# Performance work log

Measured on AMD Instinct MI355X. Metric: run time of the kernel, lower is better.

## Reference

```python
import jax, jax.numpy as jnp
import numpy as np

B, N, FD, D, HF, WF = 4, 6, 256, 128, 64, 120
IMG_H, IMG_W = 480, 960
EPS_LN = 1e-5


def bilinear_sample(fmap, pts):
    """fmap: (B,C,H,W); pts: (B,P,2) xy pixel coords. Returns (B,P,C) values
    (zeros padding, align_corners=True convention) and (B,P) in-bounds mask."""
    Bc, C, H, W = fmap.shape
    flat = fmap.reshape(Bc, C, H * W)
    x, y = pts[..., 0], pts[..., 1]
    x0, y0 = jnp.floor(x), jnp.floor(y)
    out = jnp.zeros((Bc, pts.shape[1], C), fmap.dtype)
    for dx in (0.0, 1.0):
        for dy in (0.0, 1.0):
            cx, cy = x0 + dx, y0 + dy
            wgt = (1.0 - jnp.abs(x - cx)) * (1.0 - jnp.abs(y - cy))
            inb = (cx >= 0) & (cx <= W - 1) & (cy >= 0) & (cy <= H - 1)
            idx = (jnp.clip(cy, 0, H - 1) * W + jnp.clip(cx, 0, W - 1)).astype(jnp.int32)
            g = jnp.take_along_axis(flat, idx[:, None, :], axis=2)  # (B,C,P)
            out = out + (g * (wgt * inb)[:, None, :]).transpose(0, 2, 1)
    valid = (x >= 0) & (x <= W - 1) & (y >= 0) & (y <= H - 1)
    return out, valid


def _l2norm(x, axis):
    n = jnp.sqrt(jnp.sum(x * x, axis=axis, keepdims=True))
    return x / jnp.maximum(n, 1e-12)


def _ln(x, g, b):
    mu = jnp.mean(x, axis=-1, keepdims=True)
    var = jnp.mean((x - mu) ** 2, axis=-1, keepdims=True)
    return (x - mu) / jnp.sqrt(var + EPS_LN) * g + b


def setup_inputs() -> dict:
    key = jax.random.key(0)
    ks = jax.random.split(key, 12)
    rng = np.random.RandomState(0)
    feature = jax.random.normal(ks[0], (B, N, FD, HF, WF), jnp.float32)
    # realistic intrinsics (same K family for src/tar so homographies land in-frame)
    K = np.zeros((B, N, 3, 3), np.float32)
    K[..., 0, 0] = IMG_W * 0.8 * (1 + 0.01 * rng.randn(B, N))
    K[..., 1, 1] = IMG_W * 0.8 * (1 + 0.01 * rng.randn(B, N))
    K[..., 0, 2] = IMG_W / 2
    K[..., 1, 2] = IMG_H / 2
    K[..., 2, 2] = 1.0
    I_tar_inv = np.linalg.inv(K[:, 0]).astype(np.float32)  # (B,3,3)
    # extrinsics: near-identity rotation + small translation
    E = np.tile(np.eye(4, dtype=np.float32), (B, N, 1, 1))
    w = 0.02 * rng.randn(B, N, 3).astype(np.float32)
    skew = np.zeros((B, N, 3, 3), np.float32)
    skew[..., 0, 1], skew[..., 0, 2] = -w[..., 2], w[..., 1]
    skew[..., 1, 0], skew[..., 1, 2] = w[..., 2], -w[..., 0]
    skew[..., 2, 0], skew[..., 2, 1] = -w[..., 1], w[..., 0]
    E[..., :3, :3] = np.eye(3, dtype=np.float32) + skew
    E[..., :3, 3] = 0.1 * rng.randn(B, N, 3).astype(np.float32)
    nv = np.tile(np.array([0.0, -1.0, 0.0], np.float32), (B, 1, 1))
    nv += 0.01 * rng.randn(B, 1, 3).astype(np.float32)
    nv /= np.linalg.norm(nv, axis=-1, keepdims=True)
    sc_in, sc_hid = 1.0 / np.sqrt(FD), 1.0 / np.sqrt(D)
    return {
        "feature": feature,
        "I_src": jnp.asarray(K),
        "I_tar_inv": jnp.asarray(I_tar_inv),
        "E": jnp.asarray(E),
        "dis": jnp.float32(1.5),
        "norm_vec": jnp.asarray(nv),
        "bn_gamma": jnp.ones((FD,), jnp.float32),
        "bn_beta": jnp.zeros((FD,), jnp.float32),
        "bn_mean": jnp.zeros((FD,), jnp.float32),
        "bn_var": jnp.ones((FD,), jnp.float32),
        "conv_w": jax.random.normal(ks[1], (D, FD), jnp.float32) * sc_in,
        "ln1_g": jnp.ones((D,), jnp.float32),
        "ln1_b": jnp.zeros((D,), jnp.float32),
        "mlp_w1": jax.random.normal(ks[2], (D, 2 * D), jnp.float32) * sc_hid,
        "mlp_b1": jnp.zeros((2 * D,), jnp.float32),
        "mlp_w2": jax.random.normal(ks[3], (2 * D, D), jnp.float32) * sc_hid,
        "mlp_b2": jnp.zeros((D,), jnp.float32),
        "ln2_g": jnp.ones((D,), jnp.float32),
        "ln2_b": jnp.zeros((D,), jnp.float32),
    }


def reference(feature, I_src, I_tar_inv, E, dis, norm_vec, bn_gamma, bn_beta,
              bn_mean, bn_var, conv_w, ln1_g, ln1_b, mlp_w1, mlp_b1, mlp_w2,
              mlp_b2, ln2_g, ln2_b):
    b, n, fd, h, w = feature.shape
    d = conv_w.shape[0]
    P = h * w
    # feature_linear: BN (inference stats) + ReLU + 1x1 conv (no bias)
    f = (feature - bn_mean[:, None, None]) / jnp.sqrt(bn_var[:, None, None] + 1e-5)
    f = f * bn_gamma[:, None, None] + bn_beta[:, None, None]
    f = jax.nn.relu(f)
    val = jnp.einsum('of,bnfhw->bnohw', conv_w, f)  # (b,n,d,h,w)
    # homography of normalized grid scaled to image pixels
    xs = jnp.linspace(0.0, 1.0, w)
    ys = jnp.linspace(0.0, 1.0, h)
    X, Y = jnp.meshgrid(xs, ys)  # (h,w), xy indexing
    pix = jnp.stack([X.ravel() * IMG_W, Y.ravel() * IMG_H, jnp.ones(P)], 0)  # (3,P)
    R = E[..., :3, :3]
    T = E[..., :3, 3:]
    Hm = I_src @ (R - (T @ norm_vec[:, None]) / dis) @ I_tar_inv[:, None]  # (b,n,3,3)
    homo = jnp.einsum('bnij,jp->bnip', Hm, pix.astype(Hm.dtype))
    uv = homo[:, :, :2] / homo[:, :, 2:3]
    uv = uv / jnp.array([[IMG_W], [IMG_H]], uv.dtype)  # (b,n,2,P) in ~[0,1]
    # HomoGuideAttention
    pts = (uv * jnp.array([[w], [h]], uv.dtype)).transpose(0, 1, 3, 2).reshape(b * n, P, 2)
    sampled, valid = bilinear_sample(val.reshape(b * n, d, h, w), pts)  # (bn,P,d),(bn,P)
    keyv = _l2norm(sampled, axis=2).reshape(b, n, P, d)
    query = val[:, 0]  # (b,d,h,w)
    q = _l2norm(query.reshape(b, d, P), axis=1)
    dot = jnp.einsum('bdp,bnpd->bnp', q, keyv)
    dot = dot * valid.reshape(b, n, P).astype(dot.dtype)
    att = jax.nn.softmax(dot, axis=1)
    z = jnp.einsum('bnp,bnpd->bpd', att, sampled.reshape(b, n, P, d))
    z = z.transpose(0, 2, 1).reshape(b, d, h, w) + query
    z = z.reshape(b, d, P).transpose(0, 2, 1)  # (b,P,d)
    z = _ln(z, ln1_g, ln1_b)
    hmid = jax.nn.gelu(z @ mlp_w1 + mlp_b1, approximate=False)
    z = z + (hmid @ mlp_w2 + mlp_b2)
    z = _ln(z, ln2_g, ln2_b)
    return z.transpose(0, 2, 1).reshape(b, d, h, w)
```

## Files before the change

kernel.cpp:

```cpp
#include <hip/hip_runtime.h>
#include <hip/hip_bf16.h>
#include <math.h>

#define B_ 4
#define N_ 6
#define FD_ 256
#define D_ 128
#define HF_ 64
#define WF_ 120
#define P_ (HF_*WF_)

typedef __attribute__((ext_vector_type(8))) short short8;
typedef __attribute__((ext_vector_type(4))) float floatx4;
typedef __attribute__((ext_vector_type(4))) unsigned int uint4e;

__device__ inline float gred_sum(float v) {
  v += __shfl_xor(v, 1); v += __shfl_xor(v, 2);
  v += __shfl_xor(v, 4); v += __shfl_xor(v, 8);
  return v;
}

__device__ inline unsigned short f2bf(float f) {
  unsigned int u = __builtin_bit_cast(unsigned int, f);
  u += 0x7fffu + ((u >> 16) & 1u);
  return (unsigned short)(u >> 16);
}
__device__ inline float bf2f(unsigned short h) {
  return __builtin_bit_cast(float, ((unsigned int)h) << 16);
}
__device__ inline void bfu2(unsigned int u, float& lo, float& hi) {
  lo = __builtin_bit_cast(float, u << 16);
  hi = __builtin_bit_cast(float, u & 0xffff0000u);
}

__global__ void prep_kernel(const float* __restrict__ I_src, const float* __restrict__ I_tar_inv,
                            const float* __restrict__ E, const float* __restrict__ dis,
                            const float* __restrict__ norm_vec,
                            const float* __restrict__ bn_gamma, const float* __restrict__ bn_beta,
                            const float* __restrict__ bn_mean, const float* __restrict__ bn_var,
                            float* __restrict__ bnscale, float* __restrict__ bnbias,
                            float* __restrict__ Hm) {
  int t = threadIdx.x;
  if (t < FD_) {
    float s = bn_gamma[t] * rsqrtf(bn_var[t] + 1e-5f);
    bnscale[t] = s;
    bnbias[t] = bn_beta[t] - bn_mean[t] * s;
  }
  if (t < B_*N_) {
    int b = t / N_;
    const float* e = E + t*16;
    const float* nv = norm_vec + b*3;
    float inv_dis = 1.0f / dis[0];
    float M[9];
    #pragma unroll
    for (int r = 0; r < 3; r++)
      #pragma unroll
      for (int c = 0; c < 3; c++)
        M[r*3+c] = e[r*4+c] - e[r*4+3]*nv[c]*inv_dis;
    const float* Is = I_src + t*9;
    float A[9];
    #pragma unroll
    for (int r = 0; r < 3; r++)
      #pragma unroll
      for (int c = 0; c < 3; c++)
        A[r*3+c] = Is[r*3+0]*M[0*3+c] + Is[r*3+1]*M[1*3+c] + Is[r*3+2]*M[2*3+c];
    const float* It = I_tar_inv + b*9;
    #pragma unroll
    for (int r = 0; r < 3; r++)
      #pragma unroll
      for (int c = 0; c < 3; c++)
        Hm[t*9 + r*3+c] = A[r*3+0]*It[0*3+c] + A[r*3+1]*It[1*3+c] + A[r*3+2]*It[2*3+c];
  }
}

__global__ void swizzle_w_kernel(const float* __restrict__ conv_w, unsigned short* __restrict__ wswz) {
  int t = blockIdx.x * 256 + threadIdx.x;
  int j    =  t        & 7;
  int lane = (t >> 3)  & 63;
  int dt   = (t >> 9)  & 7;
  int kc   =  t >> 12;
  int d = dt*16 + (lane & 15);
  int k = kc*32 + (lane >> 4)*8 + j;
  wswz[t] = f2bf(conv_w[d*FD_ + k]);
}

__global__ void swizzle_mlp_kernel(const float* __restrict__ w1, const float* __restrict__ w2,
                                   unsigned short* __restrict__ w1s, unsigned short* __restrict__ w2s) {
  int t = blockIdx.x * 256 + threadIdx.x;
  if (t < 32768) {
    int j    =  t        & 7;
    int lane = (t >> 3)  & 63;
    int dt   = (t >> 9)  & 15;
    int kc   =  t >> 13;
    int n = dt*16 + (lane & 15);
    int k = kc*32 + (lane >> 4)*8 + j;
    w1s[t] = f2bf(w1[k*256 + n]);
  } else {
    int u = t - 32768;
    int j    =  u        & 7;
    int lane = (u >> 3)  & 63;
    int dt   = (u >> 9)  & 7;
    int kc   =  u >> 12;
    int n = dt*16 + (lane & 15);
    int k = kc*32 + (lane >> 4)*8 + j;
    w2s[u] = f2bf(w2[k*128 + n]);
  }
}

__global__ __launch_bounds__(256) void conv_kernel(const float* __restrict__ feature,
    const unsigned short* __restrict__ wswz, const float* __restrict__ bnscale,
    const float* __restrict__ bnbias, unsigned short* __restrict__ val) {
  __shared__ unsigned short apad[2][64*36];
  __shared__ unsigned short ytile[64*136];
  __shared__ float sbn[512];

  int tid = threadIdx.x;
  if (tid < 256) { sbn[tid] = bnscale[tid]; sbn[256+tid] = bnbias[tid]; }

  int bn = blockIdx.y;
  int p0 = blockIdx.x * 64;
  const float* fbase2 = feature + (size_t)bn*FD_*P_ + p0;

  int K0 = tid >> 4;
  int pc = tid & 15;
  int sp = pc*4;

  int ln = tid & 63, wv = tid >> 6;
  int m = ln & 15, q = ln >> 4;
  int row = wv*16 + m;

  auto stage = [&](int kc, int bb) {
    int k0 = kc*32;
    const float* fb = fbase2 + (size_t)(k0 + 2*K0)*P_ + sp;
    float4 v0 = *(const float4*)fb;
    float4 v1 = *(const float4*)(fb + P_);
    float s0 = sbn[k0+2*K0],   b0 = sbn[256+k0+2*K0];
    float s1 = sbn[k0+2*K0+1], b1 = sbn[256+k0+2*K0+1];
    float a0[4] = {v0.x, v0.y, v0.z, v0.w};
    float a1[4] = {v1.x, v1.y, v1.z, v1.w};
    #pragma unroll
    for (int i = 0; i < 4; i++) {
      unsigned int w = (unsigned int)f2bf(fmaxf(a0[i]*s0+b0, 0.f))
                     | ((unsigned int)f2bf(fmaxf(a1[i]*s1+b1, 0.f)) << 16);
      *(unsigned int*)&apad[bb][(sp+i)*36 + 2*K0] = w;
    }
  };

  floatx4 acc[8];
  #pragma unroll
  for (int dt = 0; dt < 8; dt++) acc[dt] = (floatx4){0.f,0.f,0.f,0.f};

  stage(0, 0);
  __syncthreads();

  for (int kc = 0; kc < 8; kc++) {
    int bb = kc & 1;
    if (kc < 7) stage(kc+1, bb ^ 1);
    uint2 u0 = *(const uint2*)&apad[bb][row*36 + q*8];
    uint2 u1 = *(const uint2*)&apad[bb][row*36 + q*8 + 4];
    uint4e ua = {u0.x, u0.y, u1.x, u1.y};
    short8 af = __builtin_bit_cast(short8, ua);
    #pragma unroll
    for (int dt = 0; dt < 8; dt++) {
      short8 bfg = *(const short8*)(wswz + (((size_t)kc*8 + dt)*64 + ln)*8);
      acc[dt] = __builtin_amdgcn_mfma_f32_16x16x32_bf16(af, bfg, acc[dt], 0, 0, 0);
    }
    if (kc < 7) __syncthreads();
  }

  #pragma unroll
  for (int dt = 0; dt < 8; dt++)
    #pragma unroll
    for (int r = 0; r < 4; r++)
      ytile[(wv*16 + q*4 + r)*136 + dt*16 + m] = f2bf(acc[dt][r]);
  __syncthreads();
  #pragma unroll
  for (int i = 0; i < 4; i++) {
    int idx = tid + i*256;
    int pp = idx >> 4, ch = idx & 15;
    uint4 v = *(const uint4*)&ytile[pp*136 + ch*8];
    *(uint4*)(val + ((size_t)bn*P_ + p0 + pp)*D_ + ch*8) = v;
  }
}

__global__ __launch_bounds__(256) void att_kernel(const unsigned short* __restrict__ val,
    const float* __restrict__ Hm, const float* __restrict__ ln1_g,
    const float* __restrict__ ln1_b, unsigned short* __restrict__ zbuf) {
  int b = blockIdx.y;
  int p0 = blockIdx.x * 32;
  int tid = threadIdx.x;
  int ln = tid & 63, wv = tid >> 6;
  int grp = ln >> 4, c = ln & 15;

  float g1[8], be1[8];
  *(float4*)&g1[0]  = *(const float4*)(ln1_g + c*8);
  *(float4*)&g1[4]  = *(const float4*)(ln1_g + c*8 + 4);
  *(float4*)&be1[0] = *(const float4*)(ln1_b + c*8);
  *(float4*)&be1[4] = *(const float4*)(ln1_b + c*8 + 4);

  for (int pi = 0; pi < 2; pi++) {
    int p = p0 + wv*8 + grp*2 + pi;
    int py = p / WF_, px = p - py*WF_;
    float pixx = (float)px * (960.f/119.f);
    float pixy = (float)py * (480.f/63.f);

    const unsigned short* qptr = val + ((size_t)(b*N_)*P_ + p)*D_ + c*8;
    uint4 qu = *(const uint4*)qptr;
    float qv[8];
    bfu2(qu.x, qv[0], qv[1]); bfu2(qu.y, qv[2], qv[3]);
    bfu2(qu.z, qv[4], qv[5]); bfu2(qu.w, qv[6], qv[7]);
    float qp = 0.f;
    #pragma unroll
    for (int i = 0; i < 8; i++) qp += qv[i]*qv[i];
    float qinv = 1.f / fmaxf(sqrtf(gred_sum(qp)), 1e-12f);

    float dotv[N_];
    float sv[N_][8];
    #pragma unroll
    for (int n = 0; n < N_; n++) {
      const float* H = Hm + (b*N_+n)*9;
      float hx = H[0]*pixx + H[1]*pixy + H[2];
      float hy = H[3]*pixx + H[4]*pixy + H[5];
      float hz = H[6]*pixx + H[7]*pixy + H[8];
      float sx = (hx/hz) * ((float)WF_/960.f);
      float sy = (hy/hz) * ((float)HF_/480.f);
      float x0f = floorf(sx), y0f = floorf(sy);
      float fx = sx - x0f, fy = sy - y0f;
      int x0 = (int)x0f, y0 = (int)y0f;
      const unsigned short* base = val + ((size_t)(b*N_+n)*P_)*D_ + c*8;
      float acc[8];
      #pragma unroll
      for (int i = 0; i < 8; i++) acc[i] = 0.f;
      #pragma unroll
      for (int dy = 0; dy < 2; dy++) {
        #pragma unroll
        for (int dx = 0; dx < 2; dx++) {
          int cx = x0 + dx, cy = y0 + dy;
          float wgt = (dx ? fx : 1.f-fx) * (dy ? fy : 1.f-fy);
          bool inb = (cx >= 0) && (cx <= WF_-1) && (cy >= 0) && (cy <= HF_-1);
          int icx = min(max(cx,0),WF_-1), icy = min(max(cy,0),HF_-1);
          uint4 gu = *(const uint4*)(base + (size_t)(icy*WF_ + icx)*D_);
          float g[8];
          bfu2(gu.x, g[0], g[1]); bfu2(gu.y, g[2], g[3]);
          bfu2(gu.z, g[4], g[5]); bfu2(gu.w, g[6], g[7]);
          float wm = inb ? wgt : 0.f;
          #pragma unroll
          for (int i = 0; i < 8; i++) acc[i] += g[i]*wm;
        }
      }
      float ssp = 0.f, qsp = 0.f;
      #pragma unroll
      for (int i = 0; i < 8; i++) { ssp += acc[i]*acc[i]; qsp += qv[i]*acc[i]; }
      float ss = gred_sum(ssp);
      float qs = gred_sum(qsp);
      float dn = qs * qinv / fmaxf(sqrtf(ss), 1e-12f);
      bool valid = (sx >= 0.f) && (sx <= (float)(WF_-1)) && (sy >= 0.f) && (sy <= (float)(HF_-1));
      dotv[n] = valid ? dn : 0.f;
      #pragma unroll
      for (int i = 0; i < 8; i++) sv[n][i] = acc[i];
    }
    float mx = dotv[0];
    #pragma unroll
    for (int n = 1; n < N_; n++) mx = fmaxf(mx, dotv[n]);
    float e[N_]; float den = 0.f;
    #pragma unroll
    for (int n = 0; n < N_; n++) { e[n] = expf(dotv[n]-mx); den += e[n]; }
    float rden = 1.f/den;
    float z[8];
    #pragma unroll
    for (int i = 0; i < 8; i++) z[i] = qv[i];
    #pragma unroll
    for (int n = 0; n < N_; n++) {
      float a = e[n]*rden;
      #pragma unroll
      for (int i = 0; i < 8; i++) z[i] += a*sv[n][i];
    }
    float sp = 0.f;
    #pragma unroll
    for (int i = 0; i < 8; i++) sp += z[i];
    float mu = gred_sum(sp) * (1.f/128.f);
    float vp = 0.f;
    #pragma unroll
    for (int i = 0; i < 8; i++) { float d0 = z[i]-mu; vp += d0*d0; }
    float var = gred_sum(vp) * (1.f/128.f);
    float rs = rsqrtf(var + 1e-5f);
    unsigned int ow[4];
    #pragma unroll
    for (int i = 0; i < 4; i++) {
      float o0 = (z[2*i]-mu)*rs*g1[2*i] + be1[2*i];
      float o1 = (z[2*i+1]-mu)*rs*g1[2*i+1] + be1[2*i+1];
      ow[i] = (unsigned int)f2bf(o0) | ((unsigned int)f2bf(o1) << 16);
    }
    uint4 ov = make_uint4(ow[0], ow[1], ow[2], ow[3]);
    *(uint4*)(zbuf + ((size_t)b*P_ + p)*D_ + c*8) = ov;
  }
}

__global__ __launch_bounds__(256) void mlp_kernel(const unsigned short* __restrict__ zbuf,
    const unsigned short* __restrict__ w1s, const float* __restrict__ b1,
    const unsigned short* __restrict__ w2s, const float* __restrict__ b2,
    const float* __restrict__ ln2_g, const float* __restrict__ ln2_b,
    float* __restrict__ out) {
  __shared__ unsigned short zt[64*136];
  __shared__ unsigned short ht[64*264];
  int tid = threadIdx.x;
  int b = blockIdx.y;
  int p0 = blockIdx.x * 64;

  #pragma unroll
  for (int i = 0; i < 4; i++) {
    int idx = tid + i*256;
    int pp = idx >> 4, ch = idx & 15;
    uint4 v = *(const uint4*)(zbuf + ((size_t)b*P_ + p0 + pp)*D_ + ch*8);
    *(uint4*)&zt[pp*136 + ch*8] = v;
  }
  __syncthreads();

  int ln = tid & 63, wv = tid >> 6;
  int m = ln & 15, q = ln >> 4;

  floatx4 a1[16];
  #pragma unroll
  for (int dt = 0; dt < 16; dt++) a1[dt] = (floatx4){0.f,0.f,0.f,0.f};
  #pragma unroll
  for (int kc = 0; kc < 4; kc++) {
    short8 af = *(const short8*)&zt[(wv*16+m)*136 + kc*32 + q*8];
    #pragma unroll
    for (int dt = 0; dt < 16; dt++) {
      short8 bfg = *(const short8*)(w1s + (((size_t)kc*16 + dt)*64 + ln)*8);
      a1[dt] = __builtin_amdgcn_mfma_f32_16x16x32_bf16(af, bfg, a1[dt], 0, 0, 0);
    }
  }
  #pragma unroll
  for (int dt = 0; dt < 16; dt++) {
    float bb = b1[dt*16 + m];
    #pragma unroll
    for (int r = 0; r < 4; r++) {
      float x = a1[dt][r] + bb;
      float hv = 0.5f*x*(1.f + erff(x*0.70710678118654752f));
      int pp = wv*16 + q*4 + r;
      ht[pp*264 + dt*16 + m] = f2bf(hv);
    }
  }
  __syncthreads();

  floatx4 a2[8];
  #pragma unroll
  for (int dt = 0; dt < 8; dt++) a2[dt] = (floatx4){0.f,0.f,0.f,0.f};
  #pragma unroll
  for (int kc = 0; kc < 8; kc++) {
    short8 af = *(const short8*)&ht[(wv*16+m)*264 + kc*32 + q*8];
    #pragma unroll
    for (int dt = 0; dt < 8; dt++) {
      short8 bfg = *(const short8*)(w2s + (((size_t)kc*8 + dt)*64 + ln)*8);
      a2[dt] = __builtin_amdgcn_mfma_f32_16x16x32_bf16(af, bfg, a2[dt], 0, 0, 0);
    }
  }
  float y[8][4];
  #pragma unroll
  for (int dt = 0; dt < 8; dt++) {
    float bb = b2[dt*16 + m];
    #pragma unroll
    for (int r = 0; r < 4; r++) {
      int pp = wv*16 + q*4 + r;
      y[dt][r] = a2[dt][r] + bb + bf2f(zt[pp*136 + dt*16 + m]);
    }
  }
  float gg[8], be[8];
  #pragma unroll
  for (int dt = 0; dt < 8; dt++) { gg[dt] = ln2_g[dt*16+m]; be[dt] = ln2_b[dt*16+m]; }
  #pragma unroll
  for (int r = 0; r < 4; r++) {
    float sp = 0.f;
    #pragma unroll
    for (int dt = 0; dt < 8; dt++) sp += y[dt][r];
    float mu = gred_sum(sp) * (1.f/128.f);
    float vp = 0.f;
    #pragma unroll
    for (int dt = 0; dt < 8; dt++) { float d0 = y[dt][r]-mu; vp += d0*d0; }
    float rs = rsqrtf(gred_sum(vp) * (1.f/128.f) + 1e-5f);
    #pragma unroll
    for (int dt = 0; dt < 8; dt++) y[dt][r] = (y[dt][r]-mu)*rs*gg[dt] + be[dt];
  }
  __syncthreads();
  float* yt = (float*)ht;
  #pragma unroll
  for (int dt = 0; dt < 8; dt++)
    #pragma unroll
    for (int r = 0; r < 4; r++)
      yt[(dt*16 + m)*66 + wv*16 + q*4 + r] = y[dt][r];
  __syncthreads();

  #pragma unroll
  for (int i = 0; i < 16; i++) {
    int idx = tid + i*256;
    int d = idx >> 5, f2 = idx & 31;
    float2 v = *(float2*)&yt[d*66 + f2*2];
    *(float2*)(out + ((size_t)(b*D_ + d))*P_ + p0 + f2*2) = v;
  }
}

extern "C" void kernel_launch(void* const* d_in, const int* in_sizes, int n_in,
                              void* d_out, int out_size, void* d_ws, size_t ws_size,
                              hipStream_t stream) {
  (void)in_sizes; (void)n_in; (void)out_size; (void)ws_size;
  const float* feature   = (const float*)d_in[0];
  const float* I_src     = (const float*)d_in[1];
  const float* I_tar_inv = (const float*)d_in[2];
  const float* E         = (const float*)d_in[3];
  const float* dis       = (const float*)d_in[4];
  const float* norm_vec  = (const float*)d_in[5];
  const float* bn_gamma  = (const float*)d_in[6];
  const float* bn_beta   = (const float*)d_in[7];
  const float* bn_mean   = (const float*)d_in[8];
  const float* bn_var    = (const float*)d_in[9];
  const float* conv_w    = (const float*)d_in[10];
  const float* ln1_g     = (const float*)d_in[11];
  const float* ln1_b     = (const float*)d_in[12];
  const float* mlp_w1    = (const float*)d_in[13];
  const float* mlp_b1    = (const float*)d_in[14];
  const float* mlp_w2    = (const float*)d_in[15];
  const float* mlp_b2    = (const float*)d_in[16];
  const float* ln2_g     = (const float*)d_in[17];
  const float* ln2_b     = (const float*)d_in[18];
  float* out = (float*)d_out;

  char* ws = (char*)d_ws;
  float* bnscale       = (float*)(ws + 0);
  float* bnbias        = (float*)(ws + 1024);
  float* Hm            = (float*)(ws + 2048);
  unsigned short* wswz = (unsigned short*)(ws + 4096);
  unsigned short* w1s  = (unsigned short*)(ws + 69632);
  unsigned short* w2s  = (unsigned short*)(ws + 135168);
  unsigned short* val  = (unsigned short*)(ws + 200704);
  unsigned short* zbuf = (unsigned short*)(ws + 200704 + 47185920ULL);

  hipLaunchKernelGGL(prep_kernel, dim3(1), dim3(256), 0, stream,
                     I_src, I_tar_inv, E, dis, norm_vec,
                     bn_gamma, bn_beta, bn_mean, bn_var, bnscale, bnbias, Hm);
  hipLaunchKernelGGL(swizzle_w_kernel, dim3(128), dim3(256), 0, stream, conv_w, wswz);
  hipLaunchKernelGGL(swizzle_mlp_kernel, dim3(256), dim3(256), 0, stream,
                     mlp_w1, mlp_w2, w1s, w2s);
  hipLaunchKernelGGL(conv_kernel, dim3(120, 24), dim3(256), 0, stream,
                     feature, wswz, bnscale, bnbias, val);
  hipLaunchKernelGGL(att_kernel, dim3(240, 4), dim3(256), 0, stream,
                     val, Hm, ln1_g, ln1_b, zbuf);
  hipLaunchKernelGGL(mlp_kernel, dim3(120, 4), dim3(256), 0, stream,
                     zbuf, w1s, mlp_b1, w2s, mlp_b2, ln2_g, ln2_b, out);
}
```

Measured before the change: 374.4 us.

## Prefetch conv inputs two stages ahead, precompute sample coords, split MLP tiles

The conv kernel now issues global loads two k-chunks ahead in registers and aliases the output tile with the staging buffers to cut LDS use. A new uv_kernel precomputes the homography sample coordinates so the attention kernel skips per-pixel projective divides, and it batches gathers for two views at a time to raise memory-level parallelism. The MLP kernel uses 32-pixel tiles split across wave pairs, with a cross-wave LayerNorm reduction through shared memory, doubling block count. This adds an extra launch and uv buffer traffic, and uses a one-pass variance formula.

```diff
diff --git a/kernel.cpp b/kernel.cpp
--- a/kernel.cpp
+++ b/kernel.cpp
@@ -71,6 +71,22 @@
       for (int c = 0; c < 3; c++)
         Hm[t*9 + r*3+c] = A[r*3+0]*It[0*3+c] + A[r*3+1]*It[1*3+c] + A[r*3+2]*It[2*3+c];
   }
+}
+
+__global__ void uv_kernel(const float* __restrict__ Hm, float2* __restrict__ uvbuf) {
+  int t = blockIdx.x * 256 + threadIdx.x;
+  int p  = t % P_;
+  int bn = t / P_;
+  int py = p / WF_, px = p - py*WF_;
+  float pixx = (float)px * (960.f/119.f);
+  float pixy = (float)py * (480.f/63.f);
+  const float* H = Hm + bn*9;
+  float hx = H[0]*pixx + H[1]*pixy + H[2];
+  float hy = H[3]*pixx + H[4]*pixy + H[5];
+  float hz = H[6]*pixx + H[7]*pixy + H[8];
+  float sx = (hx/hz) * ((float)WF_/960.f);
+  float sy = (hy/hz) * ((float)HF_/480.f);
+  uvbuf[t] = make_float2(sx, sy);
 }
 
 __global__ void swizzle_w_kernel(const float* __restrict__ conv_w, unsigned short* __restrict__ wswz) {
@@ -107,57 +123,83 @@
   }
 }
 
+#define AST_ 36
 __global__ __launch_bounds__(256) void conv_kernel(const float* __restrict__ feature,
     const unsigned short* __restrict__ wswz, const float* __restrict__ bnscale,
     const float* __restrict__ bnbias, unsigned short* __restrict__ val) {
-  __shared__ unsigned short apad[2][64*36];
-  __shared__ unsigned short ytile[64*136];
-  __shared__ float sbn[512];
+  __shared__ __align__(16) char csm[19968];
+  unsigned short* apadA = (unsigned short*)csm;
+  unsigned short* apadB = (unsigned short*)(csm + 4608);
+  unsigned short* ytile = (unsigned short*)csm;
+  float* sbn = (float*)(csm + 17408);
 
   int tid = threadIdx.x;
-  if (tid < 256) { sbn[tid] = bnscale[tid]; sbn[256+tid] = bnbias[tid]; }
+  sbn[tid] = bnscale[tid]; sbn[256+tid] = bnbias[tid];
 
   int bn = blockIdx.y;
   int p0 = blockIdx.x * 64;
   const float* fbase2 = feature + (size_t)bn*FD_*P_ + p0;
 
   int K0 = tid >> 4;
-  int pc = tid & 15;
-  int sp = pc*4;
+  int sp = (tid & 15) * 4;
 
   int ln = tid & 63, wv = tid >> 6;
   int m = ln & 15, q = ln >> 4;
   int row = wv*16 + m;
 
-  auto stage = [&](int kc, int bb) {
-    int k0 = kc*32;
-    const float* fb = fbase2 + (size_t)(k0 + 2*K0)*P_ + sp;
-    float4 v0 = *(const float4*)fb;
-    float4 v1 = *(const float4*)(fb + P_);
+  float4 va[2], vb[2];
+  {
+    const float* fb0 = fbase2 + (size_t)(2*K0)*P_ + sp;
+    va[0] = *(const float4*)fb0; vb[0] = *(const float4*)(fb0 + P_);
+    const float* fb1 = fbase2 + (size_t)(32 + 2*K0)*P_ + sp;
+    va[1] = *(const float4*)fb1; vb[1] = *(const float4*)(fb1 + P_);
+  }
+  __syncthreads();
+
+  floatx4 acc[8];
+  #pragma unroll
+  for (int dt = 0; dt < 8; dt++) acc[dt] = (floatx4){0.f,0.f,0.f,0.f};
+
+  {
+    int k0 = 0;
     float s0 = sbn[k0+2*K0],   b0 = sbn[256+k0+2*K0];
     float s1 = sbn[k0+2*K0+1], b1 = sbn[256+k0+2*K0+1];
-    float a0[4] = {v0.x, v0.y, v0.z, v0.w};
-    float a1[4] = {v1.x, v1.y, v1.z, v1.w};
+    float a0[4] = {va[0].x, va[0].y, va[0].z, va[0].w};
+    float a1[4] = {vb[0].x, vb[0].y, vb[0].z, vb[0].w};
     #pragma unroll
     for (int i = 0; i < 4; i++) {
       unsigned int w = (unsigned int)f2bf(fmaxf(a0[i]*s0+b0, 0.f))
                      | ((unsigned int)f2bf(fmaxf(a1[i]*s1+b1, 0.f)) << 16);
-      *(unsigned int*)&apad[bb][(sp+i)*36 + 2*K0] = w;
-    }
-  };
-
-  floatx4 acc[8];
-  #pragma unroll
-  for (int dt = 0; dt < 8; dt++) acc[dt] = (floatx4){0.f,0.f,0.f,0.f};
-
-  stage(0, 0);
-  __syncthreads();
-
+      *(unsigned int*)&apadA[(sp+i)*AST_ + 2*K0] = w;
+    }
+  }
+
+  #pragma unroll
   for (int kc = 0; kc < 8; kc++) {
-    int bb = kc & 1;
-    if (kc < 7) stage(kc+1, bb ^ 1);
-    uint2 u0 = *(const uint2*)&apad[bb][row*36 + q*8];
-    uint2 u1 = *(const uint2*)&apad[bb][row*36 + q*8 + 4];
+    __syncthreads();
+    if (kc + 2 < 8) {
+      const float* fb = fbase2 + (size_t)((kc+2)*32 + 2*K0)*P_ + sp;
+      va[kc&1] = *(const float4*)fb;
+      vb[kc&1] = *(const float4*)(fb + P_);
+    }
+    if (kc + 1 < 8) {
+      int s = (kc+1)&1;
+      int k0 = (kc+1)*32;
+      unsigned short* ap = ((kc+1)&1) ? apadB : apadA;
+      float s0 = sbn[k0+2*K0],   b0 = sbn[256+k0+2*K0];
+      float s1 = sbn[k0+2*K0+1], b1 = sbn[256+k0+2*K0+1];
+      float a0[4] = {va[s].x, va[s].y, va[s].z, va[s].w};
+      float a1[4] = {vb[s].x, vb[s].y, vb[s].z, vb[s].w};
+      #pragma unroll
+      for (int i = 0; i < 4; i++) {
+        unsigned int w = (unsigned int)f2bf(fmaxf(a0[i]*s0+b0, 0.f))
+                       | ((unsigned int)f2bf(fmaxf(a1[i]*s1+b1, 0.f)) << 16);
+        *(unsigned int*)&ap[(sp+i)*AST_ + 2*K0] = w;
+      }
+    }
+    unsigned short* rp = (kc&1) ? apadB : apadA;
+    uint2 u0 = *(const uint2*)&rp[row*AST_ + q*8];
+    uint2 u1 = *(const uint2*)&rp[row*AST_ + q*8 + 4];
     uint4e ua = {u0.x, u0.y, u1.x, u1.y};
     short8 af = __builtin_bit_cast(short8, ua);
     #pragma unroll
@@ -165,8 +207,8 @@
       short8 bfg = *(const short8*)(wswz + (((size_t)kc*8 + dt)*64 + ln)*8);
       acc[dt] = __builtin_amdgcn_mfma_f32_16x16x32_bf16(af, bfg, acc[dt], 0, 0, 0);
     }
-    if (kc < 7) __syncthreads();
-  }
+  }
+  __syncthreads();
 
   #pragma unroll
   for (int dt = 0; dt < 8; dt++)
@@ -184,7 +226,7 @@
 }
 
 __global__ __launch_bounds__(256) void att_kernel(const unsigned short* __restrict__ val,
-    const float* __restrict__ Hm, const float* __restrict__ ln1_g,
+    const float2* __restrict__ uvbuf, const float* __restrict__ ln1_g,
     const float* __restrict__ ln1_b, unsigned short* __restrict__ zbuf) {
   int b = blockIdx.y;
   int p0 = blockIdx.x * 32;
@@ -200,12 +242,8 @@
 
   for (int pi = 0; pi < 2; pi++) {
     int p = p0 + wv*8 + grp*2 + pi;
-    int py = p / WF_, px = p - py*WF_;
-    float pixx = (float)px * (960.f/119.f);
-    float pixy = (float)py * (480.f/63.f);
-
-    const unsigned short* qptr = val + ((size_t)(b*N_)*P_ + p)*D_ + c*8;
-    uint4 qu = *(const uint4*)qptr;
+
+    uint4 qu = *(const uint4*)(val + ((size_t)(b*N_)*P_ + p)*D_ + c*8);
     float qv[8];
     bfu2(qu.x, qv[0], qv[1]); bfu2(qu.y, qv[2], qv[3]);
     bfu2(qu.z, qv[4], qv[5]); bfu2(qu.w, qv[6], qv[7]);
@@ -217,47 +255,53 @@
     float dotv[N_];
     float sv[N_][8];
     #pragma unroll
-    for (int n = 0; n < N_; n++) {
-      const float* H = Hm + (b*N_+n)*9;
-      float hx = H[0]*pixx + H[1]*pixy + H[2];
-      float hy = H[3]*pixx + H[4]*pixy + H[5];
-      float hz = H[6]*pixx + H[7]*pixy + H[8];
-      float sx = (hx/hz) * ((float)WF_/960.f);
-      float sy = (hy/hz) * ((float)HF_/480.f);
-      float x0f = floorf(sx), y0f = floorf(sy);
-      float fx = sx - x0f, fy = sy - y0f;
-      int x0 = (int)x0f, y0 = (int)y0f;
-      const unsigned short* base = val + ((size_t)(b*N_+n)*P_)*D_ + c*8;
-      float acc[8];
-      #pragma unroll
-      for (int i = 0; i < 8; i++) acc[i] = 0.f;
-      #pragma unroll
-      for (int dy = 0; dy < 2; dy++) {
+    for (int np = 0; np < 3; np++) {
+      uint4 g[2][4]; float wm[2][4]; bool vld[2];
+      #pragma unroll
+      for (int t = 0; t < 2; t++) {
+        int n = np*2 + t;
+        float2 uv = uvbuf[((size_t)(b*N_ + n))*P_ + p];
+        float sx = uv.x, sy = uv.y;
+        float x0f = floorf(sx), y0f = floorf(sy);
+        float fx = sx - x0f, fy = sy - y0f;
+        int x0 = (int)x0f, y0 = (int)y0f;
+        const unsigned short* base = val + ((size_t)(b*N_+n)*P_)*D_ + c*8;
         #pragma unroll
-        for (int dx = 0; dx < 2; dx++) {
+        for (int k = 0; k < 4; k++) {
+          int dx = k & 1, dy = k >> 1;
           int cx = x0 + dx, cy = y0 + dy;
-          float wgt = (dx ? fx : 1.f-fx) * (dy ? fy : 1.f-fy);
           bool inb = (cx >= 0) && (cx <= WF_-1) && (cy >= 0) && (cy <= HF_-1);
           int icx = min(max(cx,0),WF_-1), icy = min(max(cy,0),HF_-1);
-          uint4 gu = *(const uint4*)(base + (size_t)(icy*WF_ + icx)*D_);
-          float g[8];
-          bfu2(gu.x, g[0], g[1]); bfu2(gu.y, g[2], g[3]);
-          bfu2(gu.z, g[4], g[5]); bfu2(gu.w, g[6], g[7]);
-          float wm = inb ? wgt : 0.f;
+          wm[t][k] = inb ? (dx ? fx : 1.f-fx) * (dy ? fy : 1.f-fy) : 0.f;
+          g[t][k] = *(const uint4*)(base + (size_t)(icy*WF_ + icx)*D_);
+        }
+        vld[t] = (sx >= 0.f) && (sx <= (float)(WF_-1)) && (sy >= 0.f) && (sy <= (float)(HF_-1));
+      }
+      #pragma unroll
+      for (int t = 0; t < 2; t++) {
+        int n = np*2 + t;
+        float acc[8];
+        #pragma unroll
+        for (int i = 0; i < 8; i++) acc[i] = 0.f;
+        #pragma unroll
+        for (int k = 0; k < 4; k++) {
+          float gg[8];
+          bfu2(g[t][k].x, gg[0], gg[1]); bfu2(g[t][k].y, gg[2], gg[3]);
+          bfu2(g[t][k].z, gg[4], gg[5]); bfu2(g[t][k].w, gg[6], gg[7]);
+          float w = wm[t][k];
           #pragma unroll
-          for (int i = 0; i < 8; i++) acc[i] += g[i]*wm;
+          for (int i = 0; i < 8; i++) acc[i] += gg[i]*w;
         }
+        float ssp = 0.f, qsp = 0.f;
+        #pragma unroll
+        for (int i = 0; i < 8; i++) { ssp += acc[i]*acc[i]; qsp += qv[i]*acc[i]; }
+        float ss = gred_sum(ssp);
+        float qs = gred_sum(qsp);
+        float dn = qs * qinv / fmaxf(sqrtf(ss), 1e-12f);
+        dotv[n] = vld[t] ? dn : 0.f;
+        #pragma unroll
+        for (int i = 0; i < 8; i++) sv[n][i] = acc[i];
       }
-      float ssp = 0.f, qsp = 0.f;
-      #pragma unroll
-      for (int i = 0; i < 8; i++) { ssp += acc[i]*acc[i]; qsp += qv[i]*acc[i]; }
-      float ss = gred_sum(ssp);
-      float qs = gred_sum(qsp);
-      float dn = qs * qinv / fmaxf(sqrtf(ss), 1e-12f);
-      bool valid = (sx >= 0.f) && (sx <= (float)(WF_-1)) && (sy >= 0.f) && (sy <= (float)(HF_-1));
-      dotv[n] = valid ? dn : 0.f;
-      #pragma unroll
-      for (int i = 0; i < 8; i++) sv[n][i] = acc[i];
     }
     float mx = dotv[0];
     #pragma unroll
@@ -282,8 +326,7 @@
     float vp = 0.f;
     #pragma unroll
     for (int i = 0; i < 8; i++) { float d0 = z[i]-mu; vp += d0*d0; }
-    float var = gred_sum(vp) * (1.f/128.f);
-    float rs = rsqrtf(var + 1e-5f);
+    float rs = rsqrtf(gred_sum(vp) * (1.f/128.f) + 1e-5f);
     unsigned int ow[4];
     #pragma unroll
     for (int i = 0; i < 4; i++) {
@@ -291,8 +334,7 @@
       float o1 = (z[2*i+1]-mu)*rs*g1[2*i+1] + be1[2*i+1];
       ow[i] = (unsigned int)f2bf(o0) | ((unsigned int)f2bf(o1) << 16);
     }
-    uint4 ov = make_uint4(ow[0], ow[1], ow[2], ow[3]);
-    *(uint4*)(zbuf + ((size_t)b*P_ + p)*D_ + c*8) = ov;
+    *(uint4*)(zbuf + ((size_t)b*P_ + p)*D_ + c*8) = make_uint4(ow[0], ow[1], ow[2], ow[3]);
   }
 }
 
@@ -301,102 +343,124 @@
     const unsigned short* __restrict__ w2s, const float* __restrict__ b2,
     const float* __restrict__ ln2_g, const float* __restrict__ ln2_b,
     float* __restrict__ out) {
-  __shared__ unsigned short zt[64*136];
-  __shared__ unsigned short ht[64*264];
+  __shared__ __align__(16) char smem[26112];
+  unsigned short* zt = (unsigned short*)smem;
+  unsigned short* ht = (unsigned short*)(smem + 8704);
+  float* lnp = (float*)(smem + 25600);
+  float* yt = (float*)smem;
+
   int tid = threadIdx.x;
   int b = blockIdx.y;
-  int p0 = blockIdx.x * 64;
-
-  #pragma unroll
-  for (int i = 0; i < 4; i++) {
+  int p0 = blockIdx.x * 32;
+  int ln = tid & 63, wv = tid >> 6;
+  int m = ln & 15, q = ln >> 4;
+  int h = wv >> 1, ch2 = wv & 1;
+
+  #pragma unroll
+  for (int i = 0; i < 2; i++) {
     int idx = tid + i*256;
     int pp = idx >> 4, ch = idx & 15;
-    uint4 v = *(const uint4*)(zbuf + ((size_t)b*P_ + p0 + pp)*D_ + ch*8);
-    *(uint4*)&zt[pp*136 + ch*8] = v;
-  }
-  __syncthreads();
-
-  int ln = tid & 63, wv = tid >> 6;
-  int m = ln & 15, q = ln >> 4;
-
-  floatx4 a1[16];
-  #pragma unroll
-  for (int dt = 0; dt < 16; dt++) a1[dt] = (floatx4){0.f,0.f,0.f,0.f};
+    *(uint4*)&zt[pp*136 + ch*8] = *(const uint4*)(zbuf + ((size_t)b*P_ + p0 + pp)*D_ + ch*8);
+  }
+  __syncthreads();
+
+  floatx4 a1[8];
+  #pragma unroll
+  for (int j = 0; j < 8; j++) a1[j] = (floatx4){0.f,0.f,0.f,0.f};
   #pragma unroll
   for (int kc = 0; kc < 4; kc++) {
-    short8 af = *(const short8*)&zt[(wv*16+m)*136 + kc*32 + q*8];
-    #pragma unroll
-    for (int dt = 0; dt < 16; dt++) {
+    short8 af = *(const short8*)&zt[(h*16+m)*136 + kc*32 + q*8];
+    #pragma unroll
+    for (int j = 0; j < 8; j++) {
+      int dt = ch2*8 + j;
       short8 bfg = *(const short8*)(w1s + (((size_t)kc*16 + dt)*64 + ln)*8);
-      a1[dt] = __builtin_amdgcn_mfma_f32_16x16x32_bf16(af, bfg, a1[dt], 0, 0, 0);
-    }
-  }
-  #pragma unroll
-  for (int dt = 0; dt < 16; dt++) {
+      a1[j] = __builtin_amdgcn_mfma_f32_16x16x32_bf16(af, bfg, a1[j], 0, 0, 0);
+    }
+  }
+  #pragma unroll
+  for (int j = 0; j < 8; j++) {
+    int dt = ch2*8 + j;
     float bb = b1[dt*16 + m];
     #pragma unroll
     for (int r = 0; r < 4; r++) {
-      float x = a1[dt][r] + bb;
+      float x = a1[j][r] + bb;
       float hv = 0.5f*x*(1.f + erff(x*0.70710678118654752f));
-      int pp = wv*16 + q*4 + r;
-      ht[pp*264 + dt*16 + m] = f2bf(hv);
-    }
-  }
-  __syncthreads();
-
-  floatx4 a2[8];
-  #pragma unroll
-  for (int dt = 0; dt < 8; dt++) a2[dt] = (floatx4){0.f,0.f,0.f,0.f};
+      ht[(h*16 + q*4 + r)*264 + dt*16 + m] = f2bf(hv);
+    }
+  }
+  __syncthreads();
+
+  floatx4 a2[4];
+  #pragma unroll
+  for (int j = 0; j < 4; j++) a2[j] = (floatx4){0.f,0.f,0.f,0.f};
   #pragma unroll
   for (int kc = 0; kc < 8; kc++) {
-    short8 af = *(const short8*)&ht[(wv*16+m)*264 + kc*32 + q*8];
-    #pragma unroll
-    for (int dt = 0; dt < 8; dt++) {
+    short8 af = *(const short8*)&ht[(h*16+m)*264 + kc*32 + q*8];
+    #pragma unroll
+    for (int j = 0; j < 4; j++) {
+      int dt = ch2*4 + j;
       short8 bfg = *(const short8*)(w2s + (((size_t)kc*8 + dt)*64 + ln)*8);
-      a2[dt] = __builtin_amdgcn_mfma_f32_16x16x32_bf16(af, bfg, a2[dt], 0, 0, 0);
-    }
-  }
-  float y[8][4];
-  #pragma unroll
-  for (int dt = 0; dt < 8; dt++) {
+      a2[j] = __builtin_amdgcn_mfma_f32_16x16x32_bf16(af, bfg, a2[j], 0, 0, 0);
+    }
+  }
+  float y[4][4];
+  #pragma unroll
+  for (int j = 0; j < 4; j++) {
+    int dt = ch2*4 + j;
     float bb = b2[dt*16 + m];
     #pragma unroll
     for (int r = 0; r < 4; r++) {
-      int pp = wv*16 + q*4 + r;
-      y[dt][r] = a2[dt][r] + bb + bf2f(zt[pp*136 + dt*16 + m]);
-    }
-  }
-  float gg[8], be[8];
-  #pragma unroll
-  for (int dt = 0; dt < 8; dt++) { gg[dt] = ln2_g[dt*16+m]; be[dt] = ln2_b[dt*16+m]; }
+      int pp = h*16 + q*4 + r;
+      y[j][r] = a2[j][r] + bb + bf2f(zt[pp*136 + dt*16 + m]);
+    }
+  }
   #pragma unroll
   for (int r = 0; r < 4; r++) {
-    float sp = 0.f;
-    #pragma unroll
-    for (int dt = 0; dt < 8; dt++) sp += y[dt][r];
-    float mu = gred_sum(sp) * (1.f/128.f);
-    float vp = 0.f;
-    #pragma unroll
-    for (int dt = 0; dt < 8; dt++) { float d0 = y[dt][r]-mu; vp += d0*d0; }
-    float rs = rsqrtf(gred_sum(vp) * (1.f/128.f) + 1e-5f);
-    #pragma unroll
-    for (int dt = 0; dt < 8; dt++) y[dt][r] = (y[dt][r]-mu)*rs*gg[dt] + be[dt];
-  }
-  __syncthreads();
-  float* yt = (float*)ht;
-  #pragma unroll
-  for (int dt = 0; dt < 8; dt++)
+    float sp = 0.f, sq = 0.f;
+    #pragma unroll
+    for (int j = 0; j < 4; j++) { sp += y[j][r]; sq += y[j][r]*y[j][r]; }
+    sp = gred_sum(sp); sq = gred_sum(sq);
+    if (m == 0) {
+      int pl = h*16 + q*4 + r;
+      lnp[(ch2*32 + pl)*2 + 0] = sp;
+      lnp[(ch2*32 + pl)*2 + 1] = sq;
+    }
+  }
+  __syncthreads();
+  float mu_[4], rs_[4];
+  #pragma unroll
+  for (int r = 0; r < 4; r++) {
+    int pl = h*16 + q*4 + r;
+    float sum = lnp[pl*2]     + lnp[(32+pl)*2];
+    float ssq = lnp[pl*2 + 1] + lnp[(32+pl)*2 + 1];
+    float mu = sum * (1.f/128.f);
+    float var = fmaxf(ssq * (1.f/128.f) - mu*mu, 0.f);
+    mu_[r] = mu; rs_[r] = rsqrtf(var + 1e-5f);
+  }
+  float gg[4], be[4];
+  #pragma unroll
+  for (int j = 0; j < 4; j++) {
+    int d = (ch2*4 + j)*16 + m;
+    gg[j] = ln2_g[d]; be[j] = ln2_b[d];
+  }
+  #pragma unroll
+  for (int j = 0; j < 4; j++)
     #pragma unroll
     for (int r = 0; r < 4; r++)
-      yt[(dt*16 + m)*66 + wv*16 + q*4 + r] = y[dt][r];
-  __syncthreads();
-
-  #pragma unroll
-  for (int i = 0; i < 16; i++) {
+      y[j][r] = (y[j][r] - mu_[r])*rs_[r]*gg[j] + be[j];
+  __syncthreads();
+  #pragma unroll
+  for (int j = 0; j < 4; j++)
+    #pragma unroll
+    for (int r = 0; r < 4; r++)
+      yt[((ch2*4 + j)*16 + m)*34 + h*16 + q*4 + r] = y[j][r];
+  __syncthreads();
+
+  #pragma unroll
+  for (int i = 0; i < 8; i++) {
     int idx = tid + i*256;
-    int d = idx >> 5, f2 = idx & 31;
-    float2 v = *(float2*)&yt[d*66 + f2*2];
-    *(float2*)(out + ((size_t)(b*D_ + d))*P_ + p0 + f2*2) = v;
+    int d = idx >> 4, pu = idx & 15;
+    *(float2*)(out + ((size_t)(b*D_ + d))*P_ + p0 + pu*2) = *(float2*)&yt[d*34 + pu*2];
   }
 }
 
@@ -432,19 +496,21 @@
   unsigned short* wswz = (unsigned short*)(ws + 4096);
   unsigned short* w1s  = (unsigned short*)(ws + 69632);
   unsigned short* w2s  = (unsigned short*)(ws + 135168);
-  unsigned short* val  = (unsigned short*)(ws + 200704);
-  unsigned short* zbuf = (unsigned short*)(ws + 200704 + 47185920ULL);
+  float2* uvbuf        = (float2*)(ws + 200704);
+  unsigned short* val  = (unsigned short*)(ws + 1675264);
+  unsigned short* zbuf = (unsigned short*)(ws + 1675264 + 47185920ULL);
 
   hipLaunchKernelGGL(prep_kernel, dim3(1), dim3(256), 0, stream,
                      I_src, I_tar_inv, E, dis, norm_vec,
                      bn_gamma, bn_beta, bn_mean, bn_var, bnscale, bnbias, Hm);
+  hipLaunchKernelGGL(uv_kernel, dim3(720), dim3(256), 0, stream, Hm, uvbuf);
   hipLaunchKernelGGL(swizzle_w_kernel, dim3(128), dim3(256), 0, stream, conv_w, wswz);
   hipLaunchKernelGGL(swizzle_mlp_kernel, dim3(256), dim3(256), 0, stream,
                      mlp_w1, mlp_w2, w1s, w2s);
   hipLaunchKernelGGL(conv_kernel, dim3(120, 24), dim3(256), 0, stream,
                      feature, wswz, bnscale, bnbias, val);
   hipLaunchKernelGGL(att_kernel, dim3(240, 4), dim3(256), 0, stream,
-                     val, Hm, ln1_g, ln1_b, zbuf);
-  hipLaunchKernelGGL(mlp_kernel, dim3(120, 4), dim3(256), 0, stream,
+                     val, uvbuf, ln1_g, ln1_b, zbuf);
+  hipLaunchKernelGGL(mlp_kernel, dim3(240, 4), dim3(256), 0, stream,
                      zbuf, w1s, mlp_b1, w2s, mlp_b2, ln2_g, ln2_b, out);
 }
```

After: 369.1 us. No clear change (-1.4%).
